# Kernel optimization log

Measured on AMD Instinct MI355X. Metric: run time of the kernel, lower is better.

Reference implementation:

```python
import jax, jax.numpy as jnp
import numpy as np

B, S, H, NH = 2, 2048, 1024, 16
DK = H // NH

def setup_inputs() -> dict:
    key = jax.random.key(0)
    ks = jax.random.split(key, 8)
    scale = 0.02
    return {
        "x": jax.random.normal(ks[0], (B, S, H), jnp.float32),
        "mask": jax.random.randint(ks[1], (B, S, S), 0, 2, jnp.int32),
        "alibi": jax.random.normal(ks[2], (1, NH, S, S), jnp.float32),
        "W_q": jax.random.normal(ks[3], (H, H), jnp.float32) * scale,
        "b_q": jnp.zeros((H,), jnp.float32),
        "W_k": jax.random.normal(ks[4], (H, H), jnp.float32) * scale,
        "b_k": jnp.zeros((H,), jnp.float32),
        "W_v": jax.random.normal(ks[5], (H, H), jnp.float32) * scale,
        "b_v": jnp.zeros((H,), jnp.float32),
        "W_o": jax.random.normal(ks[6], (H, H), jnp.float32) * scale,
        "b_o": jnp.zeros((H,), jnp.float32),
    }

def reference(x, mask, alibi, W_q, b_q, W_k, b_k, W_v, b_v, W_o, b_o):
    b, s, h = x.shape
    def split_heads(t):  # [B,S,H] -> [B,NH,S,DK]
        return t.reshape(b, s, NH, DK).transpose(0, 2, 1, 3)
    q = split_heads(x @ W_q + b_q)
    k = split_heads(x @ W_k + b_k)
    v = split_heads(x @ W_v + b_v)
    scores = jnp.einsum("bhqd,bhkd->bhqk", q, k) / jnp.sqrt(jnp.float32(DK))
    scores = scores + alibi
    scores = jnp.where(mask[:, None, :, :] == 0, jnp.float32(-1e9), scores)
    probs = jax.nn.softmax(scores, axis=-1)  # dropout is identity in eval
    ctx = jnp.einsum("bhqk,bhkd->bhqd", probs, v)
    ctx = ctx.transpose(0, 2, 1, 3).reshape(b, s, h)
    return ctx @ W_o + b_o
```

## Files before the change

### kernel.cpp

```cpp
#include <hip/hip_runtime.h>
#include <hip/hip_bf16.h>


#define S_LEN 2048
#define H_DIM 1024
#define N_HEADS 16

typedef __bf16 bf16x8 __attribute__((ext_vector_type(8)));
typedef float f32x4 __attribute__((ext_vector_type(4)));

using gvoid = __attribute__((address_space(1))) void;
using svoid = __attribute__((address_space(3))) void;

static __device__ __forceinline__ f32x4 mfma16(bf16x8 a, bf16x8 b, f32x4 c) {
  return __builtin_amdgcn_mfma_f32_16x16x32_bf16(a, b, c, 0, 0, 0);
}

template <int NCH>
static __device__ __forceinline__ void stage64(const __bf16* g, int rstride,
                                               __bf16* lds, int wid, int lane) {
#pragma unroll
  for (int i = 0; i < NCH / 4; ++i) {
    int chunk = i * 4 + wid;
    int u = chunk * 64 + lane;
    int r = u >> 3, s = u & 7;
    const __bf16* src = g + (size_t)r * rstride + ((s ^ (r & 7)) << 3);
    __builtin_amdgcn_global_load_lds((const gvoid*)src,
                                     (svoid*)(lds + chunk * 512), 16, 0, 0);
  }
}

static __device__ __forceinline__ bf16x8 read_frag(const __bf16* lds, int r,
                                                   int slot) {
  return *(const bf16x8*)(lds + r * 64 + ((slot ^ (r & 7)) << 3));
}

static __device__ __forceinline__ ushort f2bfbits(float f) {
  unsigned u = __float_as_uint(f);
  return (ushort)((u + 0x7FFF + ((u >> 16) & 1)) >> 16);
}

__global__ __launch_bounds__(256) void k_convert_x(const float* __restrict__ x,
                                                   __bf16* __restrict__ xb) {
  size_t idx = ((size_t)blockIdx.x * 256 + threadIdx.x) * 8;
  float4 a = *(const float4*)(x + idx);
  float4 b = *(const float4*)(x + idx + 4);
  bf16x8 o;
  o[0] = (__bf16)a.x; o[1] = (__bf16)a.y; o[2] = (__bf16)a.z; o[3] = (__bf16)a.w;
  o[4] = (__bf16)b.x; o[5] = (__bf16)b.y; o[6] = (__bf16)b.z; o[7] = (__bf16)b.w;
  *(bf16x8*)(xb + idx) = o;
}

__global__ __launch_bounds__(256) void k_transpose_w(
    const float* __restrict__ w0, const float* __restrict__ w1,
    const float* __restrict__ w2, const float* __restrict__ w3,
    __bf16* __restrict__ wt) {
  __shared__ float t[64][65];
  int z = blockIdx.z;
  const float* W = (z == 0) ? w0 : (z == 1) ? w1 : (z == 2) ? w2 : w3;
  __bf16* O = wt + (size_t)z * H_DIM * H_DIM;
  int k0 = blockIdx.x * 64, n0 = blockIdx.y * 64;
  int tid = threadIdx.x;
  {
    int r = tid >> 4, c4 = tid & 15;
#pragma unroll
    for (int i = 0; i < 4; ++i) {
      float4 v = *(const float4*)(W + (size_t)(k0 + r + i * 16) * H_DIM + n0 + c4 * 4);
      t[r + i * 16][c4 * 4 + 0] = v.x;
      t[r + i * 16][c4 * 4 + 1] = v.y;
      t[r + i * 16][c4 * 4 + 2] = v.z;
      t[r + i * 16][c4 * 4 + 3] = v.w;
    }
  }
  __syncthreads();
  {
    int nn = tid >> 2, js = (tid & 3) * 16;
    bf16x8 o0, o1;
#pragma unroll
    for (int j = 0; j < 8; ++j) {
      o0[j] = (__bf16)t[js + j][nn];
      o1[j] = (__bf16)t[js + 8 + j][nn];
    }
    __bf16* dst = O + (size_t)(n0 + nn) * H_DIM + k0 + js;
    *(bf16x8*)dst = o0;
    *(bf16x8*)(dst + 8) = o1;
  }
}

__global__ __launch_bounds__(256) void k_transpose_v(const __bf16* __restrict__ V,
                                                     __bf16* __restrict__ VT) {
  __shared__ __bf16 t[64][65];
  int bh = blockIdx.y;
  int s0 = blockIdx.x * 64;
  const __bf16* Vb = V + (size_t)bh * S_LEN * 64;
  int tid = threadIdx.x;
#pragma unroll
  for (int i = 0; i < 2; ++i) {
    int u = i * 256 + tid;
    int r = u >> 3, c8 = u & 7;
    bf16x8 v = *(const bf16x8*)(Vb + (size_t)(s0 + r) * 64 + c8 * 8);
#pragma unroll
    for (int j = 0; j < 8; ++j) t[r][c8 * 8 + j] = v[j];
  }
  __syncthreads();
  int d = tid >> 2, js = (tid & 3) * 16;
  bf16x8 o0, o1;
#pragma unroll
  for (int j = 0; j < 8; ++j) {
    o0[j] = t[js + j][d];
    o1[j] = t[js + 8 + j][d];
  }
  __bf16* dst = VT + (size_t)bh * 64 * S_LEN + (size_t)d * S_LEN + s0 + js;
  *(bf16x8*)dst = o0;
  *(bf16x8*)(dst + 8) = o1;
}

template <int MODE>
__global__ __launch_bounds__(256) void k_gemm(
    const __bf16* __restrict__ A, const __bf16* __restrict__ B0,
    const __bf16* __restrict__ B1, const __bf16* __restrict__ B2,
    const float* __restrict__ bias0, const float* __restrict__ bias1,
    const float* __restrict__ bias2, __bf16* __restrict__ O0,
    __bf16* __restrict__ O1, __bf16* __restrict__ O2, float* __restrict__ Of) {
  __shared__ alignas(16) __bf16 As[128 * 64];
  __shared__ alignas(16) __bf16 Bs[128 * 64];
  int tid = threadIdx.x, wid = tid >> 6, lane = tid & 63;
  int l15 = lane & 15, lg = lane >> 4;
  int nbase = blockIdx.x * 128, mbase = blockIdx.y * 128;
  const __bf16* Bm;
  const float* bias;
  __bf16* Ob;
  if (MODE == 0) {
    int z = blockIdx.z;
    Bm = (z == 0) ? B0 : (z == 1) ? B1 : B2;
    bias = (z == 0) ? bias0 : (z == 1) ? bias1 : bias2;
    Ob = (z == 0) ? O0 : (z == 1) ? O1 : O2;
  } else {
    Bm = B0; bias = bias0; Ob = O0;
  }
  int wrow = wid >> 1, wcol = wid & 1;
  f32x4 zero = {0.f, 0.f, 0.f, 0.f};
  f32x4 acc[4][4];
#pragma unroll
  for (int i = 0; i < 4; ++i)
#pragma unroll
    for (int j = 0; j < 4; ++j) acc[i][j] = zero;

  for (int kb = 0; kb < H_DIM; kb += 64) {
    __syncthreads();
    const __bf16* Abase;
    int arstride;
    if (MODE == 0) {
      Abase = A + (size_t)mbase * H_DIM + kb;
      arstride = H_DIM;
    } else {
      int b = mbase >> 11, q0 = mbase & 2047, head = kb >> 6;
      Abase = A + ((size_t)(b * N_HEADS + head) * S_LEN + q0) * 64;
      arstride = 64;
    }
    stage64<16>(Abase, arstride, As, wid, lane);
    stage64<16>(Bm + (size_t)nbase * H_DIM + kb, H_DIM, Bs, wid, lane);
    __syncthreads();
#pragma unroll
    for (int t = 0; t < 2; ++t) {
      bf16x8 a[4], bfr[4];
#pragma unroll
      for (int i = 0; i < 4; ++i)
        a[i] = read_frag(As, wrow * 64 + i * 16 + l15, t * 4 + lg);
#pragma unroll
      for (int j = 0; j < 4; ++j)
        bfr[j] = read_frag(Bs, wcol * 64 + j * 16 + l15, t * 4 + lg);
#pragma unroll
      for (int i = 0; i < 4; ++i)
#pragma unroll
        for (int j = 0; j < 4; ++j) acc[i][j] = mfma16(a[i], bfr[j], acc[i][j]);
    }
  }
  float bv[4];
#pragma unroll
  for (int j = 0; j < 4; ++j) bv[j] = bias[nbase + wcol * 64 + j * 16 + l15];
#pragma unroll
  for (int i = 0; i < 4; ++i)
#pragma unroll
    for (int j = 0; j < 4; ++j)
#pragma unroll
      for (int r = 0; r < 4; ++r) {
        int m = mbase + wrow * 64 + i * 16 + lg * 4 + r;
        int col = nbase + wcol * 64 + j * 16 + l15;
        float v = acc[i][j][r] + bv[j];
        if (MODE == 0) {
          size_t off =
              (((size_t)(m >> 11) * N_HEADS + (col >> 6)) * S_LEN + (m & 2047)) * 64 +
              (col & 63);
          Ob[off] = (__bf16)v;
        } else {
          Of[(size_t)m * H_DIM + col] = v;
        }
      }
}

__global__ __launch_bounds__(256) void k_attn(
    const __bf16* __restrict__ Q, const __bf16* __restrict__ K,
    const __bf16* __restrict__ VT, const float* __restrict__ alibi,
    const int* __restrict__ mask, __bf16* __restrict__ ctx) {
  __shared__ alignas(16) __bf16 Ks[64 * 64];
  __shared__ alignas(16) __bf16 Vs[64 * 64];
  __shared__ alignas(16) __bf16 Ps[4][16 * 72];
  int tid = threadIdx.x, wid = tid >> 6, lane = tid & 63;
  int l15 = lane & 15, lg = lane >> 4;
  int bh = blockIdx.x;
  int b = bh & 1, h = bh >> 1;
  int qbase = blockIdx.y * 64;
  size_t bho = (size_t)(b * N_HEADS + h);
  const __bf16* Qb = Q + bho * S_LEN * 64;
  const __bf16* Kb = K + bho * S_LEN * 64;
  const __bf16* Vb = VT + bho * 64 * S_LEN;

  bf16x8 qa[2];
  {
    const __bf16* qrow = Qb + (size_t)(qbase + wid * 16 + l15) * 64;
    qa[0] = *(const bf16x8*)(qrow + lg * 8);
    qa[1] = *(const bf16x8*)(qrow + 32 + lg * 8);
  }
  float mrun[4], lrun[4];
  f32x4 cacc[4];
  f32x4 zero = {0.f, 0.f, 0.f, 0.f};
#pragma unroll
  for (int r = 0; r < 4; ++r) {
    mrun[r] = -__builtin_inff();
    lrun[r] = 0.f;
    cacc[r] = zero;
  }
  const float* abase[4];
  const int* mbase_[4];
#pragma unroll
  for (int r = 0; r < 4; ++r) {
    int q = qbase + wid * 16 + lg * 4 + r;
    abase[r] = alibi + ((size_t)h * S_LEN + q) * S_LEN + l15;
    mbase_[r] = mask + ((size_t)b * S_LEN + q) * S_LEN + l15;
  }

  for (int kt = 0; kt < S_LEN; kt += 64) {
    __syncthreads();
    stage64<8>(Kb + (size_t)kt * 64, 64, Ks, wid, lane);
    stage64<8>(Vb + kt, S_LEN, Vs, wid, lane);
    __syncthreads();

    float alb[4][4];
    int msk[4][4];
#pragma unroll
    for (int r = 0; r < 4; ++r)
#pragma unroll
      for (int c = 0; c < 4; ++c) {
        alb[r][c] = abase[r][kt + c * 16];
        msk[r][c] = mbase_[r][kt + c * 16];
      }

    f32x4 sacc[4];
#pragma unroll
    for (int c = 0; c < 4; ++c) sacc[c] = zero;
#pragma unroll
    for (int t = 0; t < 2; ++t) {
      bf16x8 kf[4];
#pragma unroll
      for (int c = 0; c < 4; ++c) kf[c] = read_frag(Ks, c * 16 + l15, t * 4 + lg);
#pragma unroll
      for (int c = 0; c < 4; ++c) sacc[c] = mfma16(qa[t], kf[c], sacc[c]);
    }

    float p[4][4], tmax[4];
#pragma unroll
    for (int r = 0; r < 4; ++r) {
      tmax[r] = -__builtin_inff();
#pragma unroll
      for (int c = 0; c < 4; ++c) {
        float s = msk[r][c] ? sacc[c][r] * 0.125f + alb[r][c] : -1e9f;
        p[r][c] = s;
        tmax[r] = fmaxf(tmax[r], s);
      }
#pragma unroll
      for (int xm = 1; xm < 16; xm <<= 1)
        tmax[r] = fmaxf(tmax[r], __shfl_xor(tmax[r], xm));
    }
    float scl[4];
#pragma unroll
    for (int r = 0; r < 4; ++r) {
      float mn = fmaxf(mrun[r], tmax[r]);
      scl[r] = __expf(mrun[r] - mn);
      mrun[r] = mn;
      float rs = 0.f;
#pragma unroll
      for (int c = 0; c < 4; ++c) {
        float pe = __expf(p[r][c] - mn);
        p[r][c] = pe;
        rs += pe;
      }
#pragma unroll
      for (int xm = 1; xm < 16; xm <<= 1) rs += __shfl_xor(rs, xm);
      lrun[r] = lrun[r] * scl[r] + rs;
    }
#pragma unroll
    for (int c = 0; c < 4; ++c) {
      f32x4 v = cacc[c];
      v[0] *= scl[0]; v[1] *= scl[1]; v[2] *= scl[2]; v[3] *= scl[3];
      cacc[c] = v;
    }
#pragma unroll
    for (int r = 0; r < 4; ++r)
#pragma unroll
      for (int c = 0; c < 4; ++c)
        Ps[wid][(lg * 4 + r) * 72 + c * 16 + l15] = (__bf16)p[r][c];
#pragma unroll
    for (int t = 0; t < 2; ++t) {
      bf16x8 pa = *(const bf16x8*)(&Ps[wid][l15 * 72 + t * 32 + lg * 8]);
#pragma unroll
      for (int c = 0; c < 4; ++c) {
        bf16x8 vb = read_frag(Vs, c * 16 + l15, t * 4 + lg);
        cacc[c] = mfma16(pa, vb, cacc[c]);
      }
    }
  }
#pragma unroll
  for (int c = 0; c < 4; ++c)
#pragma unroll
    for (int r = 0; r < 4; ++r) {
      int q = qbase + wid * 16 + lg * 4 + r;
      int d = c * 16 + l15;
      ctx[bho * S_LEN * 64 + (size_t)q * 64 + d] = (__bf16)(cacc[c][r] / lrun[r]);
    }
}

extern "C" void kernel_launch(void* const* d_in, const int* in_sizes, int n_in,
                              void* d_out, int out_size, void* d_ws,
                              size_t ws_size, hipStream_t stream) {
  const float* x = (const float*)d_in[0];
  const int* mask = (const int*)d_in[1];
  const float* alibi = (const float*)d_in[2];
  const float* Wq = (const float*)d_in[3];
  const float* bq = (const float*)d_in[4];
  const float* Wk = (const float*)d_in[5];
  const float* bk = (const float*)d_in[6];
  const float* Wv = (const float*)d_in[7];
  const float* bv = (const float*)d_in[8];
  const float* Wo = (const float*)d_in[9];
  const float* bo = (const float*)d_in[10];
  float* out = (float*)d_out;
  char* ws = (char*)d_ws;

  const size_t MB = 1u << 20;
  __bf16* xb = (__bf16*)(ws);
  __bf16* wt = (__bf16*)(ws + 8 * MB);
  __bf16* Qb = (__bf16*)(ws + 16 * MB);
  __bf16* Kb = (__bf16*)(ws + 24 * MB);
  __bf16* Vb = (__bf16*)(ws + 32 * MB);
  __bf16* VTb = (__bf16*)(ws + 40 * MB);
  __bf16* ctxb = xb;
  __bf16* wtq = wt;
  __bf16* wtk = wt + (1u << 20);
  __bf16* wtv = wt + 2 * (1u << 20);
  __bf16* wto = wt + 3 * (1u << 20);

  k_convert_x<<<dim3(2048), 256, 0, stream>>>(x, xb);
  k_transpose_w<<<dim3(16, 16, 4), 256, 0, stream>>>(Wq, Wk, Wv, Wo, wt);
  k_gemm<0><<<dim3(8, 32, 3), 256, 0, stream>>>(xb, wtq, wtk, wtv, bq, bk, bv,
                                                Qb, Kb, Vb, nullptr);
  k_transpose_v<<<dim3(32, 32), 256, 0, stream>>>(Vb, VTb);
  k_attn<<<dim3(32, 32), 256, 0, stream>>>(Qb, Kb, VTb, alibi, mask, ctxb);
  k_gemm<1><<<dim3(8, 32, 1), 256, 0, stream>>>(ctxb, wto, nullptr, nullptr, bo,
                                                nullptr, nullptr, nullptr,
                                                nullptr, nullptr, out);
}
```

Before: 280.5 us.

## Bit-pack mask, double-buffer K/V tiles, fold softmax scale into Q projection

Adds a kernel that packs the int32 attention mask into 64-bit ballot words, so the attention kernel reads one word per row per tile instead of 16 ints per thread. The K/V LDS tiles are double-buffered, and alibi and mask values are prefetched one tile ahead, so global loads overlap with the MFMA and softmax work and one barrier per iteration is removed. The 1/sqrt(dk) scale is folded into the Q projection epilogue. The pack kernel still reads the full 32 MB mask once, and LDS use for K/V doubles.

```diff
diff --git a/kernel.cpp b/kernel.cpp
--- a/kernel.cpp
+++ b/kernel.cpp
@@ -33,11 +33,6 @@
 static __device__ __forceinline__ bf16x8 read_frag(const __bf16* lds, int r,
                                                    int slot) {
   return *(const bf16x8*)(lds + r * 64 + ((slot ^ (r & 7)) << 3));
-}
-
-static __device__ __forceinline__ ushort f2bfbits(float f) {
-  unsigned u = __float_as_uint(f);
-  return (ushort)((u + 0x7FFF + ((u >> 16) & 1)) >> 16);
 }
 
 __global__ __launch_bounds__(256) void k_convert_x(const float* __restrict__ x,
@@ -113,6 +108,13 @@
   __bf16* dst = VT + (size_t)bh * 64 * S_LEN + (size_t)d * S_LEN + s0 + js;
   *(bf16x8*)dst = o0;
   *(bf16x8*)(dst + 8) = o1;
+}
+
+__global__ __launch_bounds__(256) void k_pack_mask(
+    const int* __restrict__ m, unsigned long long* __restrict__ out) {
+  size_t idx = (size_t)blockIdx.x * 256 + threadIdx.x;
+  unsigned long long b = __ballot(m[idx] != 0);
+  if ((threadIdx.x & 63) == 0) out[idx >> 6] = b;
 }
 
 template <int MODE>
@@ -130,11 +132,13 @@
   const __bf16* Bm;
   const float* bias;
   __bf16* Ob;
+  float oscale = 1.0f;
   if (MODE == 0) {
     int z = blockIdx.z;
     Bm = (z == 0) ? B0 : (z == 1) ? B1 : B2;
     bias = (z == 0) ? bias0 : (z == 1) ? bias1 : bias2;
     Ob = (z == 0) ? O0 : (z == 1) ? O1 : O2;
+    if (z == 0) oscale = 0.125f;
   } else {
     Bm = B0; bias = bias0; Ob = O0;
   }
@@ -187,7 +191,7 @@
       for (int r = 0; r < 4; ++r) {
         int m = mbase + wrow * 64 + i * 16 + lg * 4 + r;
         int col = nbase + wcol * 64 + j * 16 + l15;
-        float v = acc[i][j][r] + bv[j];
+        float v = (acc[i][j][r] + bv[j]) * oscale;
         if (MODE == 0) {
           size_t off =
               (((size_t)(m >> 11) * N_HEADS + (col >> 6)) * S_LEN + (m & 2047)) * 64 +
@@ -202,9 +206,9 @@
 __global__ __launch_bounds__(256) void k_attn(
     const __bf16* __restrict__ Q, const __bf16* __restrict__ K,
     const __bf16* __restrict__ VT, const float* __restrict__ alibi,
-    const int* __restrict__ mask, __bf16* __restrict__ ctx) {
-  __shared__ alignas(16) __bf16 Ks[64 * 64];
-  __shared__ alignas(16) __bf16 Vs[64 * 64];
+    const unsigned long long* __restrict__ maskb, __bf16* __restrict__ ctx) {
+  __shared__ alignas(16) __bf16 Ks[2][64 * 64];
+  __shared__ alignas(16) __bf16 Vs[2][64 * 64];
   __shared__ alignas(16) __bf16 Ps[4][16 * 72];
   int tid = threadIdx.x, wid = tid >> 6, lane = tid & 63;
   int l15 = lane & 15, lg = lane >> 4;
@@ -232,49 +236,69 @@
     cacc[r] = zero;
   }
   const float* abase[4];
-  const int* mbase_[4];
+  const unsigned long long* mbb[4];
 #pragma unroll
   for (int r = 0; r < 4; ++r) {
     int q = qbase + wid * 16 + lg * 4 + r;
     abase[r] = alibi + ((size_t)h * S_LEN + q) * S_LEN + l15;
-    mbase_[r] = mask + ((size_t)b * S_LEN + q) * S_LEN + l15;
-  }
-
-  for (int kt = 0; kt < S_LEN; kt += 64) {
+    mbb[r] = maskb + ((size_t)b * S_LEN + q) * (S_LEN / 64);
+  }
+
+  float albP[16];
+  unsigned long long mskP[4];
+  auto prefetch = [&](int kt) {
+#pragma unroll
+    for (int r = 0; r < 4; ++r) {
+#pragma unroll
+      for (int c = 0; c < 4; ++c) albP[r * 4 + c] = abase[r][kt + c * 16];
+      mskP[r] = mbb[r][kt >> 6];
+    }
+  };
+
+  stage64<8>(Kb, 64, Ks[0], wid, lane);
+  stage64<8>(Vb, S_LEN, Vs[0], wid, lane);
+  prefetch(0);
+
+  for (int t = 0; t < S_LEN / 64; ++t) {
+    const int cur = t & 1;
     __syncthreads();
-    stage64<8>(Kb + (size_t)kt * 64, 64, Ks, wid, lane);
-    stage64<8>(Vb + kt, S_LEN, Vs, wid, lane);
-    __syncthreads();
-
-    float alb[4][4];
-    int msk[4][4];
-#pragma unroll
-    for (int r = 0; r < 4; ++r)
+    float albC[16];
+    unsigned long long mskC[4];
+#pragma unroll
+    for (int i = 0; i < 16; ++i) albC[i] = albP[i];
+#pragma unroll
+    for (int i = 0; i < 4; ++i) mskC[i] = mskP[i];
+    if (t + 1 < S_LEN / 64) {
+      int kn = (t + 1) * 64;
+      stage64<8>(Kb + (size_t)kn * 64, 64, Ks[cur ^ 1], wid, lane);
+      stage64<8>(Vb + kn, S_LEN, Vs[cur ^ 1], wid, lane);
+      prefetch(kn);
+    }
+
+    f32x4 sacc[4];
+#pragma unroll
+    for (int c = 0; c < 4; ++c) sacc[c] = zero;
+#pragma unroll
+    for (int t2 = 0; t2 < 2; ++t2) {
+      bf16x8 kf[4];
+#pragma unroll
+      for (int c = 0; c < 4; ++c)
+        kf[c] = read_frag(Ks[cur], c * 16 + l15, t2 * 4 + lg);
+#pragma unroll
+      for (int c = 0; c < 4; ++c) sacc[c] = mfma16(qa[t2], kf[c], sacc[c]);
+    }
+
+    float p[4][4], tmax[4];
+#pragma unroll
+    for (int r = 0; r < 4; ++r) {
+      unsigned long long sh = mskC[r] >> l15;
+      unsigned lo = (unsigned)sh, hi = (unsigned)(sh >> 32);
+      int bb[4] = {(int)(lo & 1u), (int)((lo >> 16) & 1u), (int)(hi & 1u),
+                   (int)((hi >> 16) & 1u)};
+      tmax[r] = -__builtin_inff();
 #pragma unroll
       for (int c = 0; c < 4; ++c) {
-        alb[r][c] = abase[r][kt + c * 16];
-        msk[r][c] = mbase_[r][kt + c * 16];
-      }
-
-    f32x4 sacc[4];
-#pragma unroll
-    for (int c = 0; c < 4; ++c) sacc[c] = zero;
-#pragma unroll
-    for (int t = 0; t < 2; ++t) {
-      bf16x8 kf[4];
-#pragma unroll
-      for (int c = 0; c < 4; ++c) kf[c] = read_frag(Ks, c * 16 + l15, t * 4 + lg);
-#pragma unroll
-      for (int c = 0; c < 4; ++c) sacc[c] = mfma16(qa[t], kf[c], sacc[c]);
-    }
-
-    float p[4][4], tmax[4];
-#pragma unroll
-    for (int r = 0; r < 4; ++r) {
-      tmax[r] = -__builtin_inff();
-#pragma unroll
-      for (int c = 0; c < 4; ++c) {
-        float s = msk[r][c] ? sacc[c][r] * 0.125f + alb[r][c] : -1e9f;
+        float s = bb[c] ? sacc[c][r] + albC[r * 4 + c] : -1e9f;
         p[r][c] = s;
         tmax[r] = fmaxf(tmax[r], s);
       }
@@ -311,11 +335,11 @@
       for (int c = 0; c < 4; ++c)
         Ps[wid][(lg * 4 + r) * 72 + c * 16 + l15] = (__bf16)p[r][c];
 #pragma unroll
-    for (int t = 0; t < 2; ++t) {
-      bf16x8 pa = *(const bf16x8*)(&Ps[wid][l15 * 72 + t * 32 + lg * 8]);
+    for (int t2 = 0; t2 < 2; ++t2) {
+      bf16x8 pa = *(const bf16x8*)(&Ps[wid][l15 * 72 + t2 * 32 + lg * 8]);
 #pragma unroll
       for (int c = 0; c < 4; ++c) {
-        bf16x8 vb = read_frag(Vs, c * 16 + l15, t * 4 + lg);
+        bf16x8 vb = read_frag(Vs[cur], c * 16 + l15, t2 * 4 + lg);
         cacc[c] = mfma16(pa, vb, cacc[c]);
       }
     }
@@ -359,13 +383,15 @@
   __bf16* wtk = wt + (1u << 20);
   __bf16* wtv = wt + 2 * (1u << 20);
   __bf16* wto = wt + 3 * (1u << 20);
+  unsigned long long* maskb = (unsigned long long*)Vb;
 
   k_convert_x<<<dim3(2048), 256, 0, stream>>>(x, xb);
   k_transpose_w<<<dim3(16, 16, 4), 256, 0, stream>>>(Wq, Wk, Wv, Wo, wt);
   k_gemm<0><<<dim3(8, 32, 3), 256, 0, stream>>>(xb, wtq, wtk, wtv, bq, bk, bv,
                                                 Qb, Kb, Vb, nullptr);
   k_transpose_v<<<dim3(32, 32), 256, 0, stream>>>(Vb, VTb);
-  k_attn<<<dim3(32, 32), 256, 0, stream>>>(Qb, Kb, VTb, alibi, mask, ctxb);
+  k_pack_mask<<<dim3((2 * S_LEN * S_LEN) / 256), 256, 0, stream>>>(mask, maskb);
+  k_attn<<<dim3(32, 32), 256, 0, stream>>>(Qb, Kb, VTb, alibi, maskb, ctxb);
   k_gemm<1><<<dim3(8, 32, 1), 256, 0, stream>>>(ctxb, wto, nullptr, nullptr, bo,
                                                 nullptr, nullptr, nullptr,
                                                 nullptr, nullptr, out);
```

Result: slower. 306.3 us (+9.2%).
